# Kernel tuning notes

Hardware: AMD Instinct MI355X
Metric: run time of the kernel (lower is better)

The kernel has to match this reference:

```python
import jax, jax.numpy as jnp
import numpy as np

N, F, H, D = 4096, 128, 8, 8  # nodes, in_feat, head_num, att_embedding_size
EDGE_PROB = 0.01
NEG_INF = -1e10  # original uses -10e9 * (1 - A)


def setup_inputs() -> dict:
    key = jax.random.key(0)
    k1, k2, k3, k4, k5 = jax.random.split(key, 5)
    X = jax.random.normal(k1, (N, F), dtype=jnp.float32)
    # binary dense adjacency with self-loops (faithful to the dense-mask GAT formulation)
    A = (jax.random.uniform(k2, (N, N)) < EDGE_PROB).astype(jnp.float32)
    A = jnp.maximum(A, jnp.eye(N, dtype=jnp.float32))
    W = jax.random.normal(k3, (F, H * D), dtype=jnp.float32) * 0.05
    att_self = jax.random.normal(k4, (1, H, D), dtype=jnp.float32) * 0.05
    att_neigh = jax.random.normal(k5, (1, H, D), dtype=jnp.float32) * 0.05
    bias = jnp.zeros((1, H, D), dtype=jnp.float32)
    return {"X": X, "A": A, "W": W, "att_self": att_self,
            "att_neigh": att_neigh, "bias": bias}


def reference(X, A, W, att_self, att_neigh, bias):
    # per-head linear projection: [N, H, D]
    feats = (X @ W).reshape(N, H, D)
    # attention scores a_self^T h_i and a_neigh^T h_j : [N, H]
    a_s = jnp.sum(feats * att_self, axis=-1)
    a_n = jnp.sum(feats * att_neigh, axis=-1)
    # dense logits [H, N, N]: logits[h,i,j] = a_s[i,h] + a_n[j,h]
    logits = a_s.T[:, :, None] + a_n.T[:, None, :]
    logits = jax.nn.leaky_relu(logits, 0.2)
    logits = logits + NEG_INF * (1.0 - A)[None, :, :]
    attn = jax.nn.softmax(logits, axis=-1)  # [H, N, N]
    # weighted neighbor aggregation: [N, H, D]
    out = jnp.einsum('hij,jhd->ihd', attn, feats)
    out = out + bias  # use_bias=True
    out = out.reshape(N, H * D)  # reduction='concat'
    return jax.nn.relu(out)  # activation=relu
```

## Files before the change

kernel.cpp:

```cpp
#include <hip/hip_runtime.h>
#include <hip/hip_bf16.h>

#define NNODES 4096
#define FIN    128
#define NH     8
#define HD     8
#define HDOUT  64
#define MAXNZ  1024

typedef __hip_bfloat16 bf16;

template<typename T>
__device__ __forceinline__ float ld1(const void* p, int idx) {
    if constexpr (sizeof(T) == 2) return __bfloat162float(((const bf16*)p)[idx]);
    else                          return ((const float*)p)[idx];
}
template<typename T>
__device__ __forceinline__ void st1(void* p, int idx, float v) {
    if constexpr (sizeof(T) == 2) ((bf16*)p)[idx] = __float2bfloat16(v);
    else                          ((float*)p)[idx] = v;
}

__global__ void k_detect(const void* __restrict__ A, int* __restrict__ flag) {
    *flag = ((*(const unsigned*)A & 0xFFFFu) == 0x3F80u) ? 1 : 0;
}

template<typename T>
__device__ __forceinline__ void proj_body(
    const void* X, const void* W, const void* att_s, const void* att_n,
    float* feats, float* a_s, float* a_n, int i, int t, float* xs)
{
    xs[t]      = ld1<T>(X, i * FIN + t);
    xs[t + 64] = ld1<T>(X, i * FIN + 64 + t);
    __syncthreads();

    float acc = 0.f;
    #pragma unroll 16
    for (int f = 0; f < FIN; ++f)
        acc += xs[f] * ld1<T>(W, f * HDOUT + t);

    feats[(size_t)i * HDOUT + t] = acc;

    float vs = acc * ld1<T>(att_s, t);
    float vn = acc * ld1<T>(att_n, t);
    #pragma unroll
    for (int m = 1; m < 8; m <<= 1) {
        vs += __shfl_xor(vs, m, 8);
        vn += __shfl_xor(vn, m, 8);
    }
    if ((t & 7) == 0) {
        a_s[i * NH + (t >> 3)] = vs;
        a_n[i * NH + (t >> 3)] = vn;
    }
}

__global__ __launch_bounds__(64) void k_proj(
    const int* __restrict__ flag,
    const void* __restrict__ X, const void* __restrict__ W,
    const void* __restrict__ att_s, const void* __restrict__ att_n,
    float* __restrict__ feats, float* __restrict__ a_s, float* __restrict__ a_n)
{
    __shared__ float xs[FIN];
    const int i = blockIdx.x, t = threadIdx.x;
    if (*flag) proj_body<bf16 >(X, W, att_s, att_n, feats, a_s, a_n, i, t, xs);
    else       proj_body<float>(X, W, att_s, att_n, feats, a_s, a_n, i, t, xs);
}

template<typename T>
__device__ __forceinline__ void gat_body(
    const void* A, const float* feats, const float* a_s, const float* a_n,
    const void* bias, void* out, int i, int tid,
    int* s_cnt, int* s_idx, float (*s_num)[HDOUT], float (*s_den)[HDOUT])
{
    if (tid == 0) *s_cnt = 0;
    __syncthreads();

    if constexpr (sizeof(T) == 2) {
        const ushort4* Arow = (const ushort4*)((const bf16*)A + (size_t)i * NNODES);
        #pragma unroll
        for (int it = 0; it < 4; ++it) {
            int vidx = it * 256 + tid;
            ushort4 v = Arow[vidx];
            int j0 = vidx * 4;
            if (v.x) { int p = atomicAdd(s_cnt, 1); if (p < MAXNZ) s_idx[p] = j0;     }
            if (v.y) { int p = atomicAdd(s_cnt, 1); if (p < MAXNZ) s_idx[p] = j0 + 1; }
            if (v.z) { int p = atomicAdd(s_cnt, 1); if (p < MAXNZ) s_idx[p] = j0 + 2; }
            if (v.w) { int p = atomicAdd(s_cnt, 1); if (p < MAXNZ) s_idx[p] = j0 + 3; }
        }
    } else {
        const uint4* Arow = (const uint4*)((const float*)A + (size_t)i * NNODES);
        #pragma unroll
        for (int it = 0; it < 4; ++it) {
            int vidx = it * 256 + tid;
            uint4 v = Arow[vidx];
            int j0 = vidx * 4;
            if (v.x) { int p = atomicAdd(s_cnt, 1); if (p < MAXNZ) s_idx[p] = j0;     }
            if (v.y) { int p = atomicAdd(s_cnt, 1); if (p < MAXNZ) s_idx[p] = j0 + 1; }
            if (v.z) { int p = atomicAdd(s_cnt, 1); if (p < MAXNZ) s_idx[p] = j0 + 2; }
            if (v.w) { int p = atomicAdd(s_cnt, 1); if (p < MAXNZ) s_idx[p] = j0 + 3; }
        }
    }
    __syncthreads();
    int K = *s_cnt; if (K > MAXNZ) K = MAXNZ;

    const int rep = tid >> 6;
    const int u   = tid & 63;
    const int h   = u >> 3;
    const float ash = a_s[i * NH + h];

    float num = 0.f, den = 0.f;
    for (int k = rep; k < K; k += 4) {
        int j = s_idx[k];
        float z  = ash + a_n[j * NH + h];
        float lr = (z >= 0.f) ? z : 0.2f * z;
        float e  = __expf(lr);
        float f  = feats[(size_t)j * HDOUT + u];
        num += e * f;
        den += e;
    }
    s_num[rep][u] = num;
    s_den[rep][u] = den;
    __syncthreads();

    if (tid < HDOUT) {
        float n = s_num[0][u] + s_num[1][u] + s_num[2][u] + s_num[3][u];
        float d = s_den[0][u] + s_den[1][u] + s_den[2][u] + s_den[3][u];
        float v = n / d + ld1<T>(bias, u);
        st1<T>(out, i * HDOUT + u, fmaxf(v, 0.f));
    }
}

__global__ __launch_bounds__(256) void k_gat(
    const int* __restrict__ flag,
    const void* __restrict__ A, const float* __restrict__ feats,
    const float* __restrict__ a_s, const float* __restrict__ a_n,
    const void* __restrict__ bias, void* __restrict__ out)
{
    __shared__ int   s_cnt;
    __shared__ int   s_idx[MAXNZ];
    __shared__ float s_num[4][HDOUT];
    __shared__ float s_den[4][HDOUT];
    const int i = blockIdx.x, tid = threadIdx.x;
    if (*flag) gat_body<bf16 >(A, feats, a_s, a_n, bias, out, i, tid, &s_cnt, s_idx, s_num, s_den);
    else       gat_body<float>(A, feats, a_s, a_n, bias, out, i, tid, &s_cnt, s_idx, s_num, s_den);
}

extern "C" void kernel_launch(void* const* d_in, const int* in_sizes, int n_in,
                              void* d_out, int out_size, void* d_ws, size_t ws_size,
                              hipStream_t stream) {
    const void* X     = d_in[0];
    const void* A     = d_in[1];
    const void* W     = d_in[2];
    const void* att_s = d_in[3];
    const void* att_n = d_in[4];
    const void* bias  = d_in[5];

    float* feats = (float*)d_ws;
    float* as_   = feats + (size_t)NNODES * HDOUT;
    float* an_   = as_   + (size_t)NNODES * NH;
    int*   flag  = (int*)(an_ + (size_t)NNODES * NH);

    hipLaunchKernelGGL(k_detect, dim3(1), dim3(1), 0, stream, A, flag);
    hipLaunchKernelGGL(k_proj,   dim3(NNODES), dim3(64), 0, stream,
                       flag, X, W, att_s, att_n, feats, as_, an_);
    hipLaunchKernelGGL(k_gat,    dim3(NNODES), dim3(256), 0, stream,
                       flag, A, feats, as_, an_, bias, d_out);
}
```

Measured before the change: 118.5 us.

## Fuse projection and attention into one cooperative kernel with grid sync

Replaces the detect, projection and aggregation kernels with a single cooperative kernel of 256 blocks. Each block first projects 16 nodes (4 per wavefront), then a grid-wide sync separates that phase from the sparse attention aggregation over the same 16 rows. This removes two kernel launches and the separate flag-detection kernel, which cuts launch overhead. In exchange the grid is much smaller, so there is less parallelism to hide memory latency while scanning A, and the grid barrier adds its own cost.

```diff
diff --git a/kernel.cpp b/kernel.cpp
--- a/kernel.cpp
+++ b/kernel.cpp
@@ -1,5 +1,8 @@
 #include <hip/hip_runtime.h>
+#include <hip/hip_cooperative_groups.h>
 #include <hip/hip_bf16.h>
+
+namespace cg = cooperative_groups;
 
 #define NNODES 4096
 #define FIN    128
@@ -7,6 +10,8 @@
 #define HD     8
 #define HDOUT  64
 #define MAXNZ  1024
+#define NBLK   256
+#define NPB    16
 
 typedef __hip_bfloat16 bf16;
 
@@ -21,128 +26,128 @@
     else                          ((float*)p)[idx] = v;
 }
 
-__global__ void k_detect(const void* __restrict__ A, int* __restrict__ flag) {
-    *flag = ((*(const unsigned*)A & 0xFFFFu) == 0x3F80u) ? 1 : 0;
+__device__ __forceinline__ bool a_is_bf16(const void* A) {
+    return ((*(const unsigned*)A) & 0xFFFFu) == 0x3F80u;
 }
 
+struct FusedSM {
+    float xs[4][FIN];
+    int   cnt;
+    int   idx[MAXNZ];
+    float num[4][HDOUT];
+    float den[4][HDOUT];
+};
+
 template<typename T>
-__device__ __forceinline__ void proj_body(
-    const void* X, const void* W, const void* att_s, const void* att_n,
-    float* feats, float* a_s, float* a_n, int i, int t, float* xs)
+__device__ __forceinline__ void fused_body(
+    const void* X, const void* A, const void* W,
+    const void* att_s, const void* att_n, const void* bias, void* out,
+    float* feats, float* a_s, float* a_n, FusedSM* sm)
 {
-    xs[t]      = ld1<T>(X, i * FIN + t);
-    xs[t + 64] = ld1<T>(X, i * FIN + 64 + t);
-    __syncthreads();
+    const int tid = threadIdx.x;
+    const int w   = tid >> 6;
+    const int t   = tid & 63;
 
-    float acc = 0.f;
-    #pragma unroll 16
-    for (int f = 0; f < FIN; ++f)
-        acc += xs[f] * ld1<T>(W, f * HDOUT + t);
+    for (int n = 0; n < 4; ++n) {
+        const int i = blockIdx.x * NPB + w * 4 + n;
+        sm->xs[w][t]      = ld1<T>(X, i * FIN + t);
+        sm->xs[w][t + 64] = ld1<T>(X, i * FIN + 64 + t);
+        __syncthreads();
 
-    feats[(size_t)i * HDOUT + t] = acc;
+        float acc = 0.f;
+        #pragma unroll 16
+        for (int f = 0; f < FIN; ++f)
+            acc += sm->xs[w][f] * ld1<T>(W, f * HDOUT + t);
 
-    float vs = acc * ld1<T>(att_s, t);
-    float vn = acc * ld1<T>(att_n, t);
-    #pragma unroll
-    for (int m = 1; m < 8; m <<= 1) {
-        vs += __shfl_xor(vs, m, 8);
-        vn += __shfl_xor(vn, m, 8);
+        feats[(size_t)i * HDOUT + t] = acc;
+
+        float vs = acc * ld1<T>(att_s, t);
+        float vn = acc * ld1<T>(att_n, t);
+        #pragma unroll
+        for (int m = 1; m < 8; m <<= 1) {
+            vs += __shfl_xor(vs, m, 8);
+            vn += __shfl_xor(vn, m, 8);
+        }
+        if ((t & 7) == 0) {
+            a_s[i * NH + (t >> 3)] = vs;
+            a_n[i * NH + (t >> 3)] = vn;
+        }
+        __syncthreads();
     }
-    if ((t & 7) == 0) {
-        a_s[i * NH + (t >> 3)] = vs;
-        a_n[i * NH + (t >> 3)] = vn;
+
+    cg::this_grid().sync();
+
+    for (int r = 0; r < NPB; ++r) {
+        const int i = blockIdx.x * NPB + r;
+
+        if (tid == 0) sm->cnt = 0;
+        __syncthreads();
+
+        if constexpr (sizeof(T) == 2) {
+            const ushort4* Arow = (const ushort4*)((const bf16*)A + (size_t)i * NNODES);
+            #pragma unroll
+            for (int it = 0; it < 4; ++it) {
+                int vidx = it * 256 + tid;
+                ushort4 v = Arow[vidx];
+                int j0 = vidx * 4;
+                if (v.x) { int p = atomicAdd(&sm->cnt, 1); if (p < MAXNZ) sm->idx[p] = j0;     }
+                if (v.y) { int p = atomicAdd(&sm->cnt, 1); if (p < MAXNZ) sm->idx[p] = j0 + 1; }
+                if (v.z) { int p = atomicAdd(&sm->cnt, 1); if (p < MAXNZ) sm->idx[p] = j0 + 2; }
+                if (v.w) { int p = atomicAdd(&sm->cnt, 1); if (p < MAXNZ) sm->idx[p] = j0 + 3; }
+            }
+        } else {
+            const uint4* Arow = (const uint4*)((const float*)A + (size_t)i * NNODES);
+            #pragma unroll
+            for (int it = 0; it < 4; ++it) {
+                int vidx = it * 256 + tid;
+                uint4 v = Arow[vidx];
+                int j0 = vidx * 4;
+                if (v.x) { int p = atomicAdd(&sm->cnt, 1); if (p < MAXNZ) sm->idx[p] = j0;     }
+                if (v.y) { int p = atomicAdd(&sm->cnt, 1); if (p < MAXNZ) sm->idx[p] = j0 + 1; }
+                if (v.z) { int p = atomicAdd(&sm->cnt, 1); if (p < MAXNZ) sm->idx[p] = j0 + 2; }
+                if (v.w) { int p = atomicAdd(&sm->cnt, 1); if (p < MAXNZ) sm->idx[p] = j0 + 3; }
+            }
+        }
+        __syncthreads();
+        int K = sm->cnt; if (K > MAXNZ) K = MAXNZ;
+
+        const int u = t;
+        const int h = u >> 3;
+        const float ash = a_s[i * NH + h];
+
+        float num = 0.f, den = 0.f;
+        for (int k = w; k < K; k += 4) {
+            int j = sm->idx[k];
+            float z  = ash + a_n[j * NH + h];
+            float lr = (z >= 0.f) ? z : 0.2f * z;
+            float e  = __expf(lr);
+            float f  = feats[(size_t)j * HDOUT + u];
+            num += e * f;
+            den += e;
+        }
+        sm->num[w][u] = num;
+        sm->den[w][u] = den;
+        __syncthreads();
+
+        if (tid < HDOUT) {
+            float nn = sm->num[0][u] + sm->num[1][u] + sm->num[2][u] + sm->num[3][u];
+            float dd = sm->den[0][u] + sm->den[1][u] + sm->den[2][u] + sm->den[3][u];
+            float v = nn / dd + ld1<T>(bias, u);
+            st1<T>(out, i * HDOUT + u, fmaxf(v, 0.f));
+        }
     }
 }
 
-__global__ __launch_bounds__(64) void k_proj(
-    const int* __restrict__ flag,
-    const void* __restrict__ X, const void* __restrict__ W,
-    const void* __restrict__ att_s, const void* __restrict__ att_n,
+__global__ __launch_bounds__(256) void k_fused(
+    const void* __restrict__ X, const void* __restrict__ A,
+    const void* __restrict__ W, const void* __restrict__ att_s,
+    const void* __restrict__ att_n, const void* __restrict__ bias,
+    void* __restrict__ out,
     float* __restrict__ feats, float* __restrict__ a_s, float* __restrict__ a_n)
 {
-    __shared__ float xs[FIN];
-    const int i = blockIdx.x, t = threadIdx.x;
-    if (*flag) proj_body<bf16 >(X, W, att_s, att_n, feats, a_s, a_n, i, t, xs);
-    else       proj_body<float>(X, W, att_s, att_n, feats, a_s, a_n, i, t, xs);
-}
-
-template<typename T>
-__device__ __forceinline__ void gat_body(
-    const void* A, const float* feats, const float* a_s, const float* a_n,
-    const void* bias, void* out, int i, int tid,
-    int* s_cnt, int* s_idx, float (*s_num)[HDOUT], float (*s_den)[HDOUT])
-{
-    if (tid == 0) *s_cnt = 0;
-    __syncthreads();
-
-    if constexpr (sizeof(T) == 2) {
-        const ushort4* Arow = (const ushort4*)((const bf16*)A + (size_t)i * NNODES);
-        #pragma unroll
-        for (int it = 0; it < 4; ++it) {
-            int vidx = it * 256 + tid;
-            ushort4 v = Arow[vidx];
-            int j0 = vidx * 4;
-            if (v.x) { int p = atomicAdd(s_cnt, 1); if (p < MAXNZ) s_idx[p] = j0;     }
-            if (v.y) { int p = atomicAdd(s_cnt, 1); if (p < MAXNZ) s_idx[p] = j0 + 1; }
-            if (v.z) { int p = atomicAdd(s_cnt, 1); if (p < MAXNZ) s_idx[p] = j0 + 2; }
-            if (v.w) { int p = atomicAdd(s_cnt, 1); if (p < MAXNZ) s_idx[p] = j0 + 3; }
-        }
-    } else {
-        const uint4* Arow = (const uint4*)((const float*)A + (size_t)i * NNODES);
-        #pragma unroll
-        for (int it = 0; it < 4; ++it) {
-            int vidx = it * 256 + tid;
-            uint4 v = Arow[vidx];
-            int j0 = vidx * 4;
-            if (v.x) { int p = atomicAdd(s_cnt, 1); if (p < MAXNZ) s_idx[p] = j0;     }
-            if (v.y) { int p = atomicAdd(s_cnt, 1); if (p < MAXNZ) s_idx[p] = j0 + 1; }
-            if (v.z) { int p = atomicAdd(s_cnt, 1); if (p < MAXNZ) s_idx[p] = j0 + 2; }
-            if (v.w) { int p = atomicAdd(s_cnt, 1); if (p < MAXNZ) s_idx[p] = j0 + 3; }
-        }
-    }
-    __syncthreads();
-    int K = *s_cnt; if (K > MAXNZ) K = MAXNZ;
-
-    const int rep = tid >> 6;
-    const int u   = tid & 63;
-    const int h   = u >> 3;
-    const float ash = a_s[i * NH + h];
-
-    float num = 0.f, den = 0.f;
-    for (int k = rep; k < K; k += 4) {
-        int j = s_idx[k];
-        float z  = ash + a_n[j * NH + h];
-        float lr = (z >= 0.f) ? z : 0.2f * z;
-        float e  = __expf(lr);
-        float f  = feats[(size_t)j * HDOUT + u];
-        num += e * f;
-        den += e;
-    }
-    s_num[rep][u] = num;
-    s_den[rep][u] = den;
-    __syncthreads();
-
-    if (tid < HDOUT) {
-        float n = s_num[0][u] + s_num[1][u] + s_num[2][u] + s_num[3][u];
-        float d = s_den[0][u] + s_den[1][u] + s_den[2][u] + s_den[3][u];
-        float v = n / d + ld1<T>(bias, u);
-        st1<T>(out, i * HDOUT + u, fmaxf(v, 0.f));
-    }
-}
-
-__global__ __launch_bounds__(256) void k_gat(
-    const int* __restrict__ flag,
-    const void* __restrict__ A, const float* __restrict__ feats,
-    const float* __restrict__ a_s, const float* __restrict__ a_n,
-    const void* __restrict__ bias, void* __restrict__ out)
-{
-    __shared__ int   s_cnt;
-    __shared__ int   s_idx[MAXNZ];
-    __shared__ float s_num[4][HDOUT];
-    __shared__ float s_den[4][HDOUT];
-    const int i = blockIdx.x, tid = threadIdx.x;
-    if (*flag) gat_body<bf16 >(A, feats, a_s, a_n, bias, out, i, tid, &s_cnt, s_idx, s_num, s_den);
-    else       gat_body<float>(A, feats, a_s, a_n, bias, out, i, tid, &s_cnt, s_idx, s_num, s_den);
+    __shared__ FusedSM sm;
+    if (a_is_bf16(A)) fused_body<bf16 >(X, A, W, att_s, att_n, bias, out, feats, a_s, a_n, &sm);
+    else              fused_body<float>(X, A, W, att_s, att_n, bias, out, feats, a_s, a_n, &sm);
 }
 
 extern "C" void kernel_launch(void* const* d_in, const int* in_sizes, int n_in,
@@ -158,11 +163,11 @@
     float* feats = (float*)d_ws;
     float* as_   = feats + (size_t)NNODES * HDOUT;
     float* an_   = as_   + (size_t)NNODES * NH;
-    int*   flag  = (int*)(an_ + (size_t)NNODES * NH);
+    void*  out   = d_out;
 
-    hipLaunchKernelGGL(k_detect, dim3(1), dim3(1), 0, stream, A, flag);
-    hipLaunchKernelGGL(k_proj,   dim3(NNODES), dim3(64), 0, stream,
-                       flag, X, W, att_s, att_n, feats, as_, an_);
-    hipLaunchKernelGGL(k_gat,    dim3(NNODES), dim3(256), 0, stream,
-                       flag, A, feats, as_, an_, bias, d_out);
+    void* args[] = { (void*)&X, (void*)&A, (void*)&W, (void*)&att_s,
+                     (void*)&att_n, (void*)&bias, (void*)&out,
+                     (void*)&feats, (void*)&as_, (void*)&an_ };
+    hipLaunchCooperativeKernel((const void*)k_fused, dim3(NBLK), dim3(256),
+                               args, 0, stream);
 }
```

Result: slower. 239.3 us (+102.0%).
